# Optimization experiments

Hardware: AMD Instinct MI355X
Metric: run time of the kernel (lower is better)

## Reference

```python
import jax, jax.numpy as jnp
import numpy as np

BETA = 0.25  # commitment_weight


def _conv(x, w, b=None, stride=1, pad=0):
    y = jax.lax.conv_general_dilated(x, w, (stride, stride), ((pad, pad), (pad, pad)),
                                     dimension_numbers=('NCHW', 'OIHW', 'NCHW'))
    return y if b is None else y + b[None, :, None, None]


def _convT(x, w, b):
    # PyTorch ConvTranspose2d(kernel=4, stride=2, padding=1); w stored as (in, out, 4, 4)
    wf = jnp.flip(w, (2, 3)).transpose(1, 0, 2, 3)  # -> OIHW, spatially flipped
    y = jax.lax.conv_general_dilated(x, wf, (1, 1), ((2, 2), (2, 2)), lhs_dilation=(2, 2),
                                     dimension_numbers=('NCHW', 'OIHW', 'NCHW'))
    return y + b[None, :, None, None]


def _res(x, wa, wb):
    # ResidualLayer: x + conv1x1(relu(conv3x3(x))) , both convs bias-free
    return x + _conv(jax.nn.relu(_conv(x, wa, pad=1)), wb)


def _lrelu(x):
    return jax.nn.leaky_relu(x, 0.01)


def setup_inputs() -> dict:
    key = jax.random.key(0)
    ks = iter(jax.random.split(key, 32))
    def p(shape, s=0.05):
        return jax.random.normal(next(ks), shape, jnp.float32) * s
    inp = {
        'inputs': jax.random.normal(next(ks), (16, 4, 256, 256), jnp.float32),
        # encoder
        'e1_w': p((64, 4, 4, 4)),    'e1_b': p((64,)),
        'e2_w': p((128, 64, 4, 4)),  'e2_b': p((128,)),
        'e3_w': p((128, 128, 3, 3)), 'e3_b': p((128,)),
        'r1a_w': p((128, 128, 3, 3)), 'r1b_w': p((128, 128, 1, 1)),
        'r2a_w': p((128, 128, 3, 3)), 'r2b_w': p((128, 128, 1, 1)),
        'e4_w': p((64, 128, 1, 1)),  'e4_b': p((64,)),
        # residual VQ codebooks: (num_quantizers, codebook_size, dim)
        'codebooks': p((4, 512, 64), 1.0),
        # decoder
        'd1_w': p((128, 64, 3, 3)),  'd1_b': p((128,)),
        'dr1a_w': p((128, 128, 3, 3)), 'dr1b_w': p((128, 128, 1, 1)),
        'dr2a_w': p((128, 128, 3, 3)), 'dr2b_w': p((128, 128, 1, 1)),
        'dt1_w': p((128, 64, 4, 4)), 'dt1_b': p((64,)),  # (in, out, kH, kW) torch layout
        'dt2_w': p((64, 4, 4, 4)),   'dt2_b': p((4,)),
    }
    return inp


def reference(inputs, e1_w, e1_b, e2_w, e2_b, e3_w, e3_b, r1a_w, r1b_w, r2a_w, r2b_w,
              e4_w, e4_b, codebooks, d1_w, d1_b, dr1a_w, dr1b_w, dr2a_w, dr2b_w,
              dt1_w, dt1_b, dt2_w, dt2_b):
    # ---- encoder ----
    h = _lrelu(_conv(inputs, e1_w, e1_b, 2, 1))
    h = _lrelu(_conv(h, e2_w, e2_b, 2, 1))
    h = _lrelu(_conv(h, e3_w, e3_b, 1, 1))
    h = _res(h, r1a_w, r1b_w)
    h = _res(h, r2a_w, r2b_w)
    h = _lrelu(h)
    h = _lrelu(_conv(h, e4_w, e4_b, 1, 0))
    # ---- residual vector quantization ----
    z = h.transpose(0, 2, 3, 1)                     # B,H,W,D
    B, H, W, D = z.shape
    r = z.reshape(-1, D)                            # N,D tokens
    q_out = jnp.zeros_like(r)
    idx_list, losses = [], []
    for i in range(codebooks.shape[0]):
        cb = codebooks[i]                           # K,D
        d = (r * r).sum(-1, keepdims=True) - 2.0 * (r @ cb.T) + (cb * cb).sum(-1)
        idx = jnp.argmin(d, axis=-1)                # N
        q = cb[idx]                                 # N,D gather
        losses.append(BETA * jnp.mean((jax.lax.stop_gradient(q) - r) ** 2))
        q_st = r + jax.lax.stop_gradient(q - r)     # straight-through
        q_out = q_out + q_st
        r = r - jax.lax.stop_gradient(q)            # residual for next stage
        idx_list.append(idx)
    indices = jnp.stack(idx_list, -1).reshape(B, H, W, -1)   # B,H,W,Q
    losses = jnp.stack(losses)                                # (Q,)
    qz = q_out.reshape(B, H, W, D).transpose(0, 3, 1, 2)      # B,D,H,W
    # ---- decoder ----
    h = _lrelu(_conv(qz, d1_w, d1_b, 1, 1))
    h = _res(h, dr1a_w, dr1b_w)
    h = _res(h, dr2a_w, dr2b_w)
    h = _lrelu(h)
    h = _lrelu(_convT(h, dt1_w, dt1_b))
    recons = jax.nn.relu(_convT(h, dt2_w, dt2_b))
    return recons, indices, losses
```

## Files before the change

kernel.cpp:

```cpp
#include <hip/hip_runtime.h>
#include <cstddef>


template<int ACT> __device__ __forceinline__ float actf(float v) {
    if constexpr (ACT == 1) return v > 0.f ? v : 0.f;
    else if constexpr (ACT == 2) return v > 0.f ? v : 0.01f * v;
    else return v;
}
__device__ __forceinline__ float lrelu_in(float v) { return v > 0.f ? v : 0.01f * v; }

template<int CIN, int COUT, int K, int S, int P, int HIN, int WIN, int HOUT, int WOUT,
         int ICC, int NPY, int ACT, bool BIAS>
__launch_bounds__(256, (NPY >= 4 ? 2 : 4))
__global__ void conv_k(const float* __restrict__ in, const float* __restrict__ w,
                       const float* __restrict__ bias, float* __restrict__ out)
{
    constexpr int K2 = K * K;
    constexpr int NR = S * (NPY - 1) + K;
    constexpr int BH = 16 * NPY;
    __shared__ float sw[ICC * K2 * 16];
    const int tid = threadIdx.x;
    const int tx = tid & 15, ty = tid >> 4;
    constexpr int TW = WOUT / 16;
    const int bx = blockIdx.x % TW, by = blockIdx.x / TW;
    const int ox = bx * 16 + tx;
    const int oy0 = by * BH + ty * NPY;
    const int oc0 = blockIdx.y * 16;
    const int n = blockIdx.z;
    const int ix0 = ox * S - P, iy0 = oy0 * S - P;

    int ro[NR]; float mr[NR];
#pragma unroll
    for (int r = 0; r < NR; ++r) {
        const int iy = iy0 + r;
        const bool v = (iy >= 0) && (iy < HIN);
        ro[r] = v ? iy * WIN : 0;
        mr[r] = v ? 1.f : 0.f;
    }
    int co[K]; float mc[K];
#pragma unroll
    for (int c = 0; c < K; ++c) {
        const int ix = ix0 + c;
        const bool v = (ix >= 0) && (ix < WIN);
        co[c] = v ? ix : 0;
        mc[c] = v ? 1.f : 0.f;
    }

    float acc[NPY][16];
#pragma unroll
    for (int py = 0; py < NPY; ++py)
#pragma unroll
        for (int j = 0; j < 16; ++j) acc[py][j] = 0.f;

    for (int ic0 = 0; ic0 < CIN; ic0 += ICC) {
        __syncthreads();
        for (int t = tid; t < ICC * K2 * 16; t += 256) {
            int oc_l = t & 15, r = t >> 4, k = r % K2, ic_l = r / K2;
            sw[(ic_l * K2 + k) * 16 + oc_l] =
                w[((size_t)(oc0 + oc_l) * CIN + ic0 + ic_l) * K2 + k];
        }
        __syncthreads();
#pragma unroll 1
        for (int ic_l = 0; ic_l < ICC; ++ic_l) {
            const float* ip = in + (size_t)(n * CIN + ic0 + ic_l) * HIN * WIN;
            float patch[NR][K];
#pragma unroll
            for (int r = 0; r < NR; ++r)
#pragma unroll
                for (int c = 0; c < K; ++c)
                    patch[r][c] = ip[ro[r] + co[c]] * (mr[r] * mc[c]);
            const float* swp = &sw[ic_l * K2 * 16];
#pragma unroll
            for (int ky = 0; ky < K; ++ky) {
#pragma unroll
                for (int kx = 0; kx < K; ++kx) {
                    const float4* wp = (const float4*)&swp[(ky * K + kx) * 16];
                    float4 w0 = wp[0], w1 = wp[1], w2 = wp[2], w3 = wp[3];
#pragma unroll
                    for (int py = 0; py < NPY; ++py) {
                        const float v = patch[py * S + ky][kx];
                        acc[py][0]  = fmaf(w0.x, v, acc[py][0]);
                        acc[py][1]  = fmaf(w0.y, v, acc[py][1]);
                        acc[py][2]  = fmaf(w0.z, v, acc[py][2]);
                        acc[py][3]  = fmaf(w0.w, v, acc[py][3]);
                        acc[py][4]  = fmaf(w1.x, v, acc[py][4]);
                        acc[py][5]  = fmaf(w1.y, v, acc[py][5]);
                        acc[py][6]  = fmaf(w1.z, v, acc[py][6]);
                        acc[py][7]  = fmaf(w1.w, v, acc[py][7]);
                        acc[py][8]  = fmaf(w2.x, v, acc[py][8]);
                        acc[py][9]  = fmaf(w2.y, v, acc[py][9]);
                        acc[py][10] = fmaf(w2.z, v, acc[py][10]);
                        acc[py][11] = fmaf(w2.w, v, acc[py][11]);
                        acc[py][12] = fmaf(w3.x, v, acc[py][12]);
                        acc[py][13] = fmaf(w3.y, v, acc[py][13]);
                        acc[py][14] = fmaf(w3.z, v, acc[py][14]);
                        acc[py][15] = fmaf(w3.w, v, acc[py][15]);
                    }
                }
            }
        }
    }
#pragma unroll
    for (int py = 0; py < NPY; ++py) {
#pragma unroll
        for (int j = 0; j < 16; ++j) {
            float r = acc[py][j];
            if (BIAS) r += bias[oc0 + j];
            r = actf<ACT>(r);
            out[((size_t)(n * COUT + oc0 + j) * HOUT + oy0 + py) * WOUT + ox] = r;
        }
    }
}

template<int CIN, int COUT, int NPX, int ACT, bool BIAS, bool INL, bool RESID, bool TOK>
__launch_bounds__(256, 3)
__global__ void conv1x1_k(const float* __restrict__ in, const float* __restrict__ w,
                          const float* __restrict__ bias, const float* __restrict__ resid,
                          float* __restrict__ out)
{
    constexpr int HW = 4096;
    __shared__ float sw[16 * CIN];
    const int tid = threadIdx.x;
    const int base = blockIdx.x * (256 * NPX) + tid;
    const int oc0 = blockIdx.y * 16;
    const int n = blockIdx.z;

    for (int t = tid; t < 16 * CIN; t += 256) {
        int oc_l = t & 15, ic = t >> 4;
        sw[ic * 16 + oc_l] = w[(size_t)(oc0 + oc_l) * CIN + ic];
    }
    __syncthreads();

    float acc[NPX][16];
#pragma unroll
    for (int p = 0; p < NPX; ++p)
#pragma unroll
        for (int j = 0; j < 16; ++j) acc[p][j] = 0.f;

    const float* ip = in + (size_t)n * CIN * HW;
#pragma unroll 2
    for (int ic = 0; ic < CIN; ++ic) {
        float v[NPX];
#pragma unroll
        for (int p = 0; p < NPX; ++p) {
            float t = ip[(size_t)ic * HW + base + 256 * p];
            if (INL) t = lrelu_in(t);
            v[p] = t;
        }
        const float4* wp = (const float4*)&sw[ic * 16];
#pragma unroll
        for (int q4 = 0; q4 < 4; ++q4) {
            const float4 wv = wp[q4];
#pragma unroll
            for (int p = 0; p < NPX; ++p) {
                acc[p][q4 * 4 + 0] = fmaf(wv.x, v[p], acc[p][q4 * 4 + 0]);
                acc[p][q4 * 4 + 1] = fmaf(wv.y, v[p], acc[p][q4 * 4 + 1]);
                acc[p][q4 * 4 + 2] = fmaf(wv.z, v[p], acc[p][q4 * 4 + 2]);
                acc[p][q4 * 4 + 3] = fmaf(wv.w, v[p], acc[p][q4 * 4 + 3]);
            }
        }
    }
#pragma unroll
    for (int p = 0; p < NPX; ++p) {
        const int pix = base + 256 * p;
#pragma unroll
        for (int j = 0; j < 16; ++j) {
            float r = acc[p][j];
            if (BIAS) r += bias[oc0 + j];
            r = actf<ACT>(r);
            if (RESID) r += resid[((size_t)(n * COUT + oc0 + j)) * HW + pix];
            if (TOK)
                out[((size_t)n * HW + pix) * COUT + oc0 + j] = r;
            else
                out[((size_t)(n * COUT + oc0 + j)) * HW + pix] = r;
        }
    }
}

template<int CIN, int COUT, int OCT, int HIN, int ICC, int ACT, bool INL>
__launch_bounds__(256, 3)
__global__ void convt_k(const float* __restrict__ in, const float* __restrict__ w,
                        const float* __restrict__ bias, float* __restrict__ out)
{
    constexpr int WIN = HIN, HOUT = 2 * HIN, WOUT = 2 * HIN;
    __shared__ float sw[ICC * 16 * OCT];
    const int tid = threadIdx.x;
    const int tx = tid & 15, ty = tid >> 4;
    constexpr int TBW = WOUT / 32;
    const int bx = blockIdx.x % TBW, by = blockIdx.x / TBW;
    const int A = by * 16 + ty;
    const int C = bx * 16 + tx;
    const int oc0 = blockIdx.y * OCT;
    const int n = blockIdx.z;

    int offs[9]; float msk[9];
#pragma unroll
    for (int dy = 0; dy < 3; ++dy) {
#pragma unroll
        for (int dx = 0; dx < 3; ++dx) {
            const int iy = A - 1 + dy, ix = C - 1 + dx;
            const bool v = (iy >= 0) && (iy < HIN) && (ix >= 0) && (ix < WIN);
            offs[dy * 3 + dx] = v ? iy * WIN + ix : 0;
            msk[dy * 3 + dx] = v ? 1.f : 0.f;
        }
    }

    float acc[4 * OCT];
#pragma unroll
    for (int j = 0; j < 4 * OCT; ++j) acc[j] = 0.f;

    for (int ic0 = 0; ic0 < CIN; ic0 += ICC) {
        __syncthreads();
        for (int t = tid; t < ICC * 16 * OCT; t += 256) {
            int oc_l = t % OCT, r = t / OCT, k = r & 15, ic_l = r >> 4;
            sw[(ic_l * 16 + k) * OCT + oc_l] =
                w[((size_t)(ic0 + ic_l) * COUT + oc0 + oc_l) * 16 + k];
        }
        __syncthreads();
#pragma unroll 1
        for (int ic_l = 0; ic_l < ICC; ++ic_l) {
            const float* ip = in + (size_t)(n * CIN + ic0 + ic_l) * HIN * WIN;
            float in9[9];
#pragma unroll
            for (int j = 0; j < 9; ++j) {
                float v = ip[offs[j]] * msk[j];
                if (INL) v = lrelu_in(v);
                in9[j] = v;
            }
#pragma unroll
            for (int ky = 0; ky < 4; ++ky) {
                const int ry = (ky + 1) & 1;
                const int dy = 2 - ((ky + 1) >> 1);
#pragma unroll
                for (int kx = 0; kx < 4; ++kx) {
                    const int rx = (kx + 1) & 1;
                    const int dx = 2 - ((kx + 1) >> 1);
                    const float v = in9[dy * 3 + dx];
                    const int po = ry * 2 + rx;
                    const float4* wp = (const float4*)&sw[(ic_l * 16 + ky * 4 + kx) * OCT];
#pragma unroll
                    for (int q4 = 0; q4 < OCT / 4; ++q4) {
                        float4 wv = wp[q4];
                        acc[po * OCT + q4 * 4 + 0] = fmaf(wv.x, v, acc[po * OCT + q4 * 4 + 0]);
                        acc[po * OCT + q4 * 4 + 1] = fmaf(wv.y, v, acc[po * OCT + q4 * 4 + 1]);
                        acc[po * OCT + q4 * 4 + 2] = fmaf(wv.z, v, acc[po * OCT + q4 * 4 + 2]);
                        acc[po * OCT + q4 * 4 + 3] = fmaf(wv.w, v, acc[po * OCT + q4 * 4 + 3]);
                    }
                }
            }
        }
    }
#pragma unroll
    for (int po = 0; po < 4; ++po) {
        const int ry = po >> 1, rx = po & 1;
        const int oy = 2 * A + ry, ox = 2 * C + rx;
#pragma unroll
        for (int j = 0; j < OCT; ++j) {
            float r = acc[po * OCT + j] + bias[oc0 + j];
            r = actf<ACT>(r);
            out[((size_t)(n * COUT + oc0 + j) * HOUT + oy) * WOUT + ox] = r;
        }
    }
}

__global__ void norm_k(const float* __restrict__ cb, float* __restrict__ nrm) {
    const int c = blockIdx.x * 256 + threadIdx.x;
    const float4* p = (const float4*)(cb + (size_t)c * 64);
    float a0 = 0.f, a1 = 0.f, a2 = 0.f, a3 = 0.f;
#pragma unroll
    for (int i = 0; i < 16; ++i) {
        float4 v = p[i];
        a0 = fmaf(v.x, v.x, a0); a1 = fmaf(v.y, v.y, a1);
        a2 = fmaf(v.z, v.z, a2); a3 = fmaf(v.w, v.w, a3);
    }
    nrm[c] = (a0 + a1) + (a2 + a3);
}

__launch_bounds__(128)
__global__ void rvq_k(const float* __restrict__ z, const float* __restrict__ cb,
                      const float* __restrict__ nrm,
                      float* __restrict__ q, float* __restrict__ idx_out,
                      float* __restrict__ loss_acc)
{
    __shared__ float scb[128 * 64];
    __shared__ float ssc[128];
    const int tid = threadIdx.x;
    const int h = tid & 1;
    const int tloc = tid >> 1;
    const int t = blockIdx.x * 64 + tloc;

    float zr[32], r[32];
    const float4* zp = (const float4*)(z + (size_t)t * 64 + h * 32);
#pragma unroll
    for (int i = 0; i < 8; ++i) {
        float4 v = zp[i];
        zr[4 * i + 0] = v.x; zr[4 * i + 1] = v.y; zr[4 * i + 2] = v.z; zr[4 * i + 3] = v.w;
        r[4 * i + 0] = v.x;  r[4 * i + 1] = v.y;  r[4 * i + 2] = v.z;  r[4 * i + 3] = v.w;
    }

    for (int s = 0; s < 4; ++s) {
        float s0 = 0.f, s1 = 0.f, s2 = 0.f, s3 = 0.f;
#pragma unroll
        for (int i = 0; i < 32; i += 4) {
            s0 = fmaf(r[i + 0], r[i + 0], s0);
            s1 = fmaf(r[i + 1], r[i + 1], s1);
            s2 = fmaf(r[i + 2], r[i + 2], s2);
            s3 = fmaf(r[i + 3], r[i + 3], s3);
        }
        float sr2 = (s0 + s1) + (s2 + s3);
        sr2 += __shfl_xor(sr2, 1, 64);

        float dmin = 3.4e38f;
        int best = 0;
        for (int pass = 0; pass < 4; ++pass) {
            __syncthreads();
            const float* src = cb + ((size_t)s * 512 + pass * 128) * 64;
            for (int i2 = tid; i2 < 128 * 64 / 4; i2 += 128)
                ((float4*)scb)[i2] = ((const float4*)src)[i2];
            ssc[tid] = nrm[(size_t)s * 512 + pass * 128 + tid];
            __syncthreads();
#pragma unroll 2
            for (int kk = 0; kk < 128; ++kk) {
                const float4* cp = (const float4*)&scb[kk * 64 + h * 32];
                float d0 = 0.f, d1 = 0.f, d2 = 0.f, d3 = 0.f;
#pragma unroll
                for (int i = 0; i < 8; ++i) {
                    float4 c = cp[i];
                    d0 = fmaf(r[4 * i + 0], c.x, d0);
                    d1 = fmaf(r[4 * i + 1], c.y, d1);
                    d2 = fmaf(r[4 * i + 2], c.z, d2);
                    d3 = fmaf(r[4 * i + 3], c.w, d3);
                }
                float dot = (d0 + d1) + (d2 + d3);
                dot += __shfl_xor(dot, 1, 64);
                const float d = fmaf(-2.f, dot, sr2) + ssc[kk];
                if (d < dmin) { dmin = d; best = pass * 128 + kk; }
            }
        }
        float lv = (h == 0) ? dmin : 0.f;
#pragma unroll
        for (int off = 32; off; off >>= 1) lv += __shfl_down(lv, off, 64);
        if ((tid & 63) == 0) atomicAdd(&loss_acc[s], lv);

        if (h == 0) idx_out[(size_t)t * 4 + s] = (float)best;

        const float4* cbest = (const float4*)(cb + ((size_t)s * 512 + best) * 64 + h * 32);
#pragma unroll
        for (int i = 0; i < 8; ++i) {
            float4 c = cbest[i];
            r[4 * i + 0] -= c.x; r[4 * i + 1] -= c.y;
            r[4 * i + 2] -= c.z; r[4 * i + 3] -= c.w;
        }
    }
    const int n = t >> 12, pix = t & 4095;
    float* qp = q + (size_t)n * 64 * 4096 + pix;
#pragma unroll
    for (int i = 0; i < 32; ++i)
        qp[(size_t)(h * 32 + i) * 4096] = zr[i] - r[i];
}

__global__ void init_k(float* loss_acc) {
    if (threadIdx.x < 4) loss_acc[threadIdx.x] = 0.f;
}
__global__ void fin_k(const float* __restrict__ loss_acc, float* __restrict__ out_loss) {
    if (threadIdx.x < 4)
        out_loss[threadIdx.x] = loss_acc[threadIdx.x] * (0.25f / 4194304.f);
}

extern "C" void kernel_launch(void* const* d_in, const int* in_sizes, int n_in,
                              void* d_out, int out_size, void* d_ws, size_t ws_size,
                              hipStream_t stream)
{
    const float* x    = (const float*)d_in[0];
    const float* e1w  = (const float*)d_in[1];  const float* e1b = (const float*)d_in[2];
    const float* e2w  = (const float*)d_in[3];  const float* e2b = (const float*)d_in[4];
    const float* e3w  = (const float*)d_in[5];  const float* e3b = (const float*)d_in[6];
    const float* r1aw = (const float*)d_in[7];  const float* r1bw = (const float*)d_in[8];
    const float* r2aw = (const float*)d_in[9];  const float* r2bw = (const float*)d_in[10];
    const float* e4w  = (const float*)d_in[11]; const float* e4b = (const float*)d_in[12];
    const float* cbs  = (const float*)d_in[13];
    const float* d1w  = (const float*)d_in[14]; const float* d1b = (const float*)d_in[15];
    const float* dr1aw= (const float*)d_in[16]; const float* dr1bw = (const float*)d_in[17];
    const float* dr2aw= (const float*)d_in[18]; const float* dr2bw = (const float*)d_in[19];
    const float* dt1w = (const float*)d_in[20]; const float* dt1b = (const float*)d_in[21];
    const float* dt2w = (const float*)d_in[22]; const float* dt2b = (const float*)d_in[23];

    float* out = (float*)d_out;
    float* ws  = (float*)d_ws;

    float* BIG = ws;
    float* P2  = BIG;
    float* P3  = BIG + 8388608;
    float* P1  = ws + 16777216;
    float* Z   = ws + 25165824;
    float* Q   = ws + 29360128;
    float* LACC= ws + 33554432;
    float* NRM = ws + 33554448;

    float* out_recons = out;
    float* out_idx    = out + 4194304;
    float* out_loss   = out + 4194304 + 262144;

    init_k<<<1, 64, 0, stream>>>(LACC);
    norm_k<<<8, 256, 0, stream>>>(cbs, NRM);

    conv_k<4, 64, 4, 2, 1, 256, 256, 128, 128, 4, 1, 2, true>
        <<<dim3(64, 4, 16), 256, 0, stream>>>(x, e1w, e1b, BIG);
    conv_k<64, 128, 4, 2, 1, 128, 128, 64, 64, 16, 2, 2, true>
        <<<dim3(8, 8, 16), 256, 0, stream>>>(BIG, e2w, e2b, P1);
    conv_k<128, 128, 3, 1, 1, 64, 64, 64, 64, 16, 4, 2, true>
        <<<dim3(4, 8, 16), 256, 0, stream>>>(P1, e3w, e3b, P2);
    conv_k<128, 128, 3, 1, 1, 64, 64, 64, 64, 16, 4, 1, false>
        <<<dim3(4, 8, 16), 256, 0, stream>>>(P2, r1aw, nullptr, P3);
    conv1x1_k<128, 128, 4, 0, false, false, true, false>
        <<<dim3(4, 8, 16), 256, 0, stream>>>(P3, r1bw, nullptr, P2, P1);
    conv_k<128, 128, 3, 1, 1, 64, 64, 64, 64, 16, 4, 1, false>
        <<<dim3(4, 8, 16), 256, 0, stream>>>(P1, r2aw, nullptr, P3);
    conv1x1_k<128, 128, 4, 0, false, false, true, false>
        <<<dim3(4, 8, 16), 256, 0, stream>>>(P3, r2bw, nullptr, P1, P2);
    conv1x1_k<128, 64, 2, 2, true, true, false, true>
        <<<dim3(8, 4, 16), 256, 0, stream>>>(P2, e4w, e4b, nullptr, Z);

    rvq_k<<<1024, 128, 0, stream>>>(Z, cbs, NRM, Q, out_idx, LACC);
    fin_k<<<1, 64, 0, stream>>>(LACC, out_loss);

    conv_k<64, 128, 3, 1, 1, 64, 64, 64, 64, 16, 4, 2, true>
        <<<dim3(4, 8, 16), 256, 0, stream>>>(Q, d1w, d1b, P1);
    conv_k<128, 128, 3, 1, 1, 64, 64, 64, 64, 16, 4, 1, false>
        <<<dim3(4, 8, 16), 256, 0, stream>>>(P1, dr1aw, nullptr, P2);
    conv1x1_k<128, 128, 4, 0, false, false, true, false>
        <<<dim3(4, 8, 16), 256, 0, stream>>>(P2, dr1bw, nullptr, P1, P3);
    conv_k<128, 128, 3, 1, 1, 64, 64, 64, 64, 16, 4, 1, false>
        <<<dim3(4, 8, 16), 256, 0, stream>>>(P3, dr2aw, nullptr, P2);
    conv1x1_k<128, 128, 4, 0, false, false, true, false>
        <<<dim3(4, 8, 16), 256, 0, stream>>>(P2, dr2bw, nullptr, P3, P1);
    convt_k<128, 64, 16, 64, 8, 2, true>
        <<<dim3(16, 4, 16), 256, 0, stream>>>(P1, dt1w, dt1b, BIG);
    convt_k<64, 4, 4, 128, 16, 1, false>
        <<<dim3(64, 1, 16), 256, 0, stream>>>(BIG, dt2w, dt2b, out_recons);
}
```

Measured before the change: 2.858 ms.

## Drop shared-memory staging in 3x3, 1x1 convs and RVQ; read weights directly

```diff
diff --git a/kernel.cpp b/kernel.cpp
--- a/kernel.cpp
+++ b/kernel.cpp
@@ -112,6 +112,84 @@
     }
 }
 
+template<int CIN, int ACT, bool BIAS>
+__launch_bounds__(256, 2)
+__global__ void conv3d_k(const float* __restrict__ in, const float* __restrict__ w,
+                         const float* __restrict__ bias, float* __restrict__ out)
+{
+    constexpr int H = 64, W = 64, COUT = 128, NPY = 4, NR = NPY + 2;
+    const int tid = threadIdx.x;
+    const int tx = tid & 15, ty = tid >> 4;
+    const int bx = blockIdx.x & 3, by = blockIdx.x >> 2;
+    const int ox = bx * 16 + tx;
+    const int oy0 = by * 64 + ty * NPY;
+    const int oc0 = blockIdx.y * 16;
+    const int n = blockIdx.z;
+    const int ix0 = ox - 1, iy0 = oy0 - 1;
+
+    int ro[NR]; float mr[NR];
+#pragma unroll
+    for (int r = 0; r < NR; ++r) {
+        const int iy = iy0 + r;
+        const bool v = (iy >= 0) && (iy < H);
+        ro[r] = v ? iy * W : 0;
+        mr[r] = v ? 1.f : 0.f;
+    }
+    int co[3]; float mc[3];
+#pragma unroll
+    for (int c = 0; c < 3; ++c) {
+        const int ix = ix0 + c;
+        const bool v = (ix >= 0) && (ix < W);
+        co[c] = v ? ix : 0;
+        mc[c] = v ? 1.f : 0.f;
+    }
+
+    float acc[NPY][16];
+#pragma unroll
+    for (int py = 0; py < NPY; ++py)
+#pragma unroll
+        for (int j = 0; j < 16; ++j) acc[py][j] = 0.f;
+
+#pragma unroll 1
+    for (int ic = 0; ic < CIN; ++ic) {
+        const float* ip = in + (size_t)(n * CIN + ic) * H * W;
+        float patch[NR][3];
+#pragma unroll
+        for (int r = 0; r < NR; ++r)
+#pragma unroll
+            for (int c = 0; c < 3; ++c)
+                patch[r][c] = ip[ro[r] + co[c]] * (mr[r] * mc[c]);
+#pragma unroll
+        for (int ky = 0; ky < 3; ++ky) {
+#pragma unroll
+            for (int kx = 0; kx < 3; ++kx) {
+                const int kk = ky * 3 + kx;
+                float wv[16];
+#pragma unroll
+                for (int j = 0; j < 16; ++j)
+                    wv[j] = w[((size_t)(oc0 + j) * CIN + ic) * 9 + kk];
+#pragma unroll
+                for (int py = 0; py < NPY; ++py) {
+                    const float v = patch[py + ky][kx];
+#pragma unroll
+                    for (int j = 0; j < 16; ++j)
+                        acc[py][j] = fmaf(wv[j], v, acc[py][j]);
+                }
+            }
+        }
+    }
+#pragma unroll
+    for (int py = 0; py < NPY; ++py) {
+#pragma unroll
+        for (int j = 0; j < 16; ++j) {
+            float r = acc[py][j];
+            if (BIAS) r += bias[oc0 + j];
+            r = actf<ACT>(r);
+            out[((size_t)(n * COUT + oc0 + j) * H + oy0 + py) * W + ox] = r;
+        }
+    }
+}
+
 template<int CIN, int COUT, int NPX, int ACT, bool BIAS, bool INL, bool RESID, bool TOK>
 __launch_bounds__(256, 3)
 __global__ void conv1x1_k(const float* __restrict__ in, const float* __restrict__ w,
@@ -119,18 +197,11 @@
                           float* __restrict__ out)
 {
     constexpr int HW = 4096;
-    __shared__ float sw[16 * CIN];
     const int tid = threadIdx.x;
     const int base = blockIdx.x * (256 * NPX) + tid;
     const int oc0 = blockIdx.y * 16;
     const int n = blockIdx.z;
 
-    for (int t = tid; t < 16 * CIN; t += 256) {
-        int oc_l = t & 15, ic = t >> 4;
-        sw[ic * 16 + oc_l] = w[(size_t)(oc0 + oc_l) * CIN + ic];
-    }
-    __syncthreads();
-
     float acc[NPX][16];
 #pragma unroll
     for (int p = 0; p < NPX; ++p)
@@ -147,18 +218,15 @@
             if (INL) t = lrelu_in(t);
             v[p] = t;
         }
-        const float4* wp = (const float4*)&sw[ic * 16];
-#pragma unroll
-        for (int q4 = 0; q4 < 4; ++q4) {
-            const float4 wv = wp[q4];
-#pragma unroll
-            for (int p = 0; p < NPX; ++p) {
-                acc[p][q4 * 4 + 0] = fmaf(wv.x, v[p], acc[p][q4 * 4 + 0]);
-                acc[p][q4 * 4 + 1] = fmaf(wv.y, v[p], acc[p][q4 * 4 + 1]);
-                acc[p][q4 * 4 + 2] = fmaf(wv.z, v[p], acc[p][q4 * 4 + 2]);
-                acc[p][q4 * 4 + 3] = fmaf(wv.w, v[p], acc[p][q4 * 4 + 3]);
-            }
-        }
+        float wv[16];
+#pragma unroll
+        for (int j = 0; j < 16; ++j)
+            wv[j] = w[(size_t)(oc0 + j) * CIN + ic];
+#pragma unroll
+        for (int j = 0; j < 16; ++j)
+#pragma unroll
+            for (int p = 0; p < NPX; ++p)
+                acc[p][j] = fmaf(wv[j], v[p], acc[p][j]);
     }
 #pragma unroll
     for (int p = 0; p < NPX; ++p) {
@@ -276,87 +344,86 @@
     nrm[c] = (a0 + a1) + (a2 + a3);
 }
 
-__launch_bounds__(128)
-__global__ void rvq_k(const float* __restrict__ z, const float* __restrict__ cb,
-                      const float* __restrict__ nrm,
-                      float* __restrict__ q, float* __restrict__ idx_out,
-                      float* __restrict__ loss_acc)
+__launch_bounds__(256)
+__global__ void rvq3_k(const float* __restrict__ z, const float* __restrict__ cb,
+                       const float* __restrict__ nrm,
+                       float* __restrict__ q, float* __restrict__ idx_out,
+                       float* __restrict__ loss_acc)
 {
-    __shared__ float scb[128 * 64];
-    __shared__ float ssc[128];
     const int tid = threadIdx.x;
-    const int h = tid & 1;
-    const int tloc = tid >> 1;
-    const int t = blockIdx.x * 64 + tloc;
-
-    float zr[32], r[32];
-    const float4* zp = (const float4*)(z + (size_t)t * 64 + h * 32);
-#pragma unroll
-    for (int i = 0; i < 8; ++i) {
-        float4 v = zp[i];
-        zr[4 * i + 0] = v.x; zr[4 * i + 1] = v.y; zr[4 * i + 2] = v.z; zr[4 * i + 3] = v.w;
-        r[4 * i + 0] = v.x;  r[4 * i + 1] = v.y;  r[4 * i + 2] = v.z;  r[4 * i + 3] = v.w;
+    const int t = blockIdx.x * 256 + tid;
+
+    float r[64];
+    {
+        const float4* zp = (const float4*)(z + (size_t)t * 64);
+#pragma unroll
+        for (int i = 0; i < 16; ++i) {
+            float4 v = zp[i];
+            r[4 * i + 0] = v.x; r[4 * i + 1] = v.y;
+            r[4 * i + 2] = v.z; r[4 * i + 3] = v.w;
+        }
     }
 
     for (int s = 0; s < 4; ++s) {
         float s0 = 0.f, s1 = 0.f, s2 = 0.f, s3 = 0.f;
 #pragma unroll
-        for (int i = 0; i < 32; i += 4) {
+        for (int i = 0; i < 64; i += 4) {
             s0 = fmaf(r[i + 0], r[i + 0], s0);
             s1 = fmaf(r[i + 1], r[i + 1], s1);
             s2 = fmaf(r[i + 2], r[i + 2], s2);
             s3 = fmaf(r[i + 3], r[i + 3], s3);
         }
-        float sr2 = (s0 + s1) + (s2 + s3);
-        sr2 += __shfl_xor(sr2, 1, 64);
+        const float sr2 = (s0 + s1) + (s2 + s3);
 
         float dmin = 3.4e38f;
         int best = 0;
-        for (int pass = 0; pass < 4; ++pass) {
-            __syncthreads();
-            const float* src = cb + ((size_t)s * 512 + pass * 128) * 64;
-            for (int i2 = tid; i2 < 128 * 64 / 4; i2 += 128)
-                ((float4*)scb)[i2] = ((const float4*)src)[i2];
-            ssc[tid] = nrm[(size_t)s * 512 + pass * 128 + tid];
-            __syncthreads();
+        const float* cbs_ = cb + (size_t)s * 512 * 64;
+        const float* nr_ = nrm + s * 512;
 #pragma unroll 2
-            for (int kk = 0; kk < 128; ++kk) {
-                const float4* cp = (const float4*)&scb[kk * 64 + h * 32];
-                float d0 = 0.f, d1 = 0.f, d2 = 0.f, d3 = 0.f;
-#pragma unroll
-                for (int i = 0; i < 8; ++i) {
-                    float4 c = cp[i];
-                    d0 = fmaf(r[4 * i + 0], c.x, d0);
-                    d1 = fmaf(r[4 * i + 1], c.y, d1);
-                    d2 = fmaf(r[4 * i + 2], c.z, d2);
-                    d3 = fmaf(r[4 * i + 3], c.w, d3);
-                }
-                float dot = (d0 + d1) + (d2 + d3);
-                dot += __shfl_xor(dot, 1, 64);
-                const float d = fmaf(-2.f, dot, sr2) + ssc[kk];
-                if (d < dmin) { dmin = d; best = pass * 128 + kk; }
+        for (int kk = 0; kk < 512; ++kk) {
+            const float4* cp = (const float4*)(cbs_ + (size_t)kk * 64);
+            float d0 = 0.f, d1 = 0.f, d2 = 0.f, d3 = 0.f;
+#pragma unroll
+            for (int i = 0; i < 16; ++i) {
+                const float4 c = cp[i];
+                d0 = fmaf(r[4 * i + 0], c.x, d0);
+                d1 = fmaf(r[4 * i + 1], c.y, d1);
+                d2 = fmaf(r[4 * i + 2], c.z, d2);
+                d3 = fmaf(r[4 * i + 3], c.w, d3);
             }
-        }
-        float lv = (h == 0) ? dmin : 0.f;
+            const float dot = (d0 + d1) + (d2 + d3);
+            const float d = fmaf(-2.f, dot, sr2) + nr_[kk];
+            if (d < dmin) { dmin = d; best = kk; }
+        }
+
+        float lv = dmin;
 #pragma unroll
         for (int off = 32; off; off >>= 1) lv += __shfl_down(lv, off, 64);
         if ((tid & 63) == 0) atomicAdd(&loss_acc[s], lv);
 
-        if (h == 0) idx_out[(size_t)t * 4 + s] = (float)best;
-
-        const float4* cbest = (const float4*)(cb + ((size_t)s * 512 + best) * 64 + h * 32);
-#pragma unroll
-        for (int i = 0; i < 8; ++i) {
-            float4 c = cbest[i];
+        idx_out[(size_t)t * 4 + s] = (float)best;
+
+        const float4* cbest = (const float4*)(cbs_ + (size_t)best * 64);
+#pragma unroll
+        for (int i = 0; i < 16; ++i) {
+            const float4 c = cbest[i];
             r[4 * i + 0] -= c.x; r[4 * i + 1] -= c.y;
             r[4 * i + 2] -= c.z; r[4 * i + 3] -= c.w;
         }
     }
-    const int n = t >> 12, pix = t & 4095;
-    float* qp = q + (size_t)n * 64 * 4096 + pix;
-#pragma unroll
-    for (int i = 0; i < 32; ++i)
-        qp[(size_t)(h * 32 + i) * 4096] = zr[i] - r[i];
+    {
+        const int n = t >> 12, pix = t & 4095;
+        float* qp = q + (size_t)n * 64 * 4096 + pix;
+        const float4* zp = (const float4*)(z + (size_t)t * 64);
+#pragma unroll
+        for (int i = 0; i < 16; ++i) {
+            const float4 v = zp[i];
+            qp[(size_t)(4 * i + 0) * 4096] = v.x - r[4 * i + 0];
+            qp[(size_t)(4 * i + 1) * 4096] = v.y - r[4 * i + 1];
+            qp[(size_t)(4 * i + 2) * 4096] = v.z - r[4 * i + 2];
+            qp[(size_t)(4 * i + 3) * 4096] = v.w - r[4 * i + 3];
+        }
+    }
 }
 
 __global__ void init_k(float* loss_acc) {
@@ -408,29 +475,29 @@
         <<<dim3(64, 4, 16), 256, 0, stream>>>(x, e1w, e1b, BIG);
     conv_k<64, 128, 4, 2, 1, 128, 128, 64, 64, 16, 2, 2, true>
         <<<dim3(8, 8, 16), 256, 0, stream>>>(BIG, e2w, e2b, P1);
-    conv_k<128, 128, 3, 1, 1, 64, 64, 64, 64, 16, 4, 2, true>
+    conv3d_k<128, 2, true>
         <<<dim3(4, 8, 16), 256, 0, stream>>>(P1, e3w, e3b, P2);
-    conv_k<128, 128, 3, 1, 1, 64, 64, 64, 64, 16, 4, 1, false>
+    conv3d_k<128, 1, false>
         <<<dim3(4, 8, 16), 256, 0, stream>>>(P2, r1aw, nullptr, P3);
     conv1x1_k<128, 128, 4, 0, false, false, true, false>
         <<<dim3(4, 8, 16), 256, 0, stream>>>(P3, r1bw, nullptr, P2, P1);
-    conv_k<128, 128, 3, 1, 1, 64, 64, 64, 64, 16, 4, 1, false>
+    conv3d_k<128, 1, false>
         <<<dim3(4, 8, 16), 256, 0, stream>>>(P1, r2aw, nullptr, P3);
     conv1x1_k<128, 128, 4, 0, false, false, true, false>
         <<<dim3(4, 8, 16), 256, 0, stream>>>(P3, r2bw, nullptr, P1, P2);
     conv1x1_k<128, 64, 2, 2, true, true, false, true>
         <<<dim3(8, 4, 16), 256, 0, stream>>>(P2, e4w, e4b, nullptr, Z);
 
-    rvq_k<<<1024, 128, 0, stream>>>(Z, cbs, NRM, Q, out_idx, LACC);
+    rvq3_k<<<256, 256, 0, stream>>>(Z, cbs, NRM, Q, out_idx, LACC);
     fin_k<<<1, 64, 0, stream>>>(LACC, out_loss);
 
-    conv_k<64, 128, 3, 1, 1, 64, 64, 64, 64, 16, 4, 2, true>
+    conv3d_k<64, 2, true>
         <<<dim3(4, 8, 16), 256, 0, stream>>>(Q, d1w, d1b, P1);
-    conv_k<128, 128, 3, 1, 1, 64, 64, 64, 64, 16, 4, 1, false>
+    conv3d_k<128, 1, false>
         <<<dim3(4, 8, 16), 256, 0, stream>>>(P1, dr1aw, nullptr, P2);
     conv1x1_k<128, 128, 4, 0, false, false, true, false>
         <<<dim3(4, 8, 16), 256, 0, stream>>>(P2, dr1bw, nullptr, P1, P3);
-    conv_k<128, 128, 3, 1, 1, 64, 64, 64, 64, 16, 4, 1, false>
+    conv3d_k<128, 1, false>
         <<<dim3(4, 8, 16), 256, 0, stream>>>(P3, dr2aw, nullptr, P2);
     conv1x1_k<128, 128, 4, 0, false, false, true, false>
         <<<dim3(4, 8, 16), 256, 0, stream>>>(P2, dr2bw, nullptr, P3, P1);
```

New measurement: 3.848 ms. 34.6% more time.
